# Kernel optimization log

Measured on AMD Instinct MI355X. Metric: run time of the kernel, lower is better.

The kernel has to match this reference:

```python
import jax, jax.numpy as jnp
import numpy as np
from jax import lax

B, C, N = 128, 320, 256
H = W = 16
GROUPS = 5
RATIO = 8
MASK_EPS = 1e-6   # registered buffer 'eps' in the torch module
GN_EPS = 1e-5     # torch GroupNorm default


def setup_inputs() -> dict:
    key = jax.random.key(0)
    ks = jax.random.split(key, 10)
    def rn(k, shape, scale=0.05):
        return jax.random.normal(k, shape, dtype=jnp.float32) * scale
    return {
        "x": jax.random.normal(ks[0], (B, C, N), dtype=jnp.float32),
        "low_cutoff": jnp.float32(0.2),
        "high_cutoff": jnp.float32(0.7),
        "ca_w1": rn(ks[1], (C // RATIO, C)),
        "ca_b1": jnp.zeros((C // RATIO,), jnp.float32),
        "ca_w2": rn(ks[2], (3 * C, C // RATIO)),
        "ca_b2": jnp.zeros((3 * C,), jnp.float32),
        "low_w": rn(ks[3], (C, C, 3, 3)),
        "low_b": jnp.zeros((C,), jnp.float32),
        "low_g": jnp.ones((C,), jnp.float32),
        "low_beta": jnp.zeros((C,), jnp.float32),
        "mid_w": rn(ks[4], (C, C, 3, 3)),
        "mid_b": jnp.zeros((C,), jnp.float32),
        "mid_g": jnp.ones((C,), jnp.float32),
        "mid_beta": jnp.zeros((C,), jnp.float32),
        "high_w": rn(ks[5], (C, C, 3, 3)),
        "high_b": jnp.zeros((C,), jnp.float32),
        "high_g": jnp.ones((C,), jnp.float32),
        "high_beta": jnp.zeros((C,), jnp.float32),
        "sa_w": rn(ks[6], (1, C, 1, 1)),
        "sa_b": jnp.zeros((1,), jnp.float32),
    }


def _conv3x3_gn(y, w, b, gamma, beta):
    # Conv2d(C,C,3,padding=1) -> GroupNorm(5,C)
    out = lax.conv_general_dilated(
        y, w, window_strides=(1, 1), padding='SAME',
        dimension_numbers=('NCHW', 'OIHW', 'NCHW'))
    out = out + b[None, :, None, None]
    b_, c_, h_, w_ = out.shape
    g = out.reshape(b_, GROUPS, c_ // GROUPS, h_, w_)
    mu = g.mean(axis=(2, 3, 4), keepdims=True)
    var = g.var(axis=(2, 3, 4), keepdims=True)
    g = (g - mu) * lax.rsqrt(var + GN_EPS)
    out = g.reshape(b_, c_, h_, w_)
    return out * gamma[None, :, None, None] + beta[None, :, None, None]


def reference(x, low_cutoff, high_cutoff, ca_w1, ca_b1, ca_w2, ca_b2,
              low_w, low_b, low_g, low_beta,
              mid_w, mid_b, mid_g, mid_beta,
              high_w, high_b, high_g, high_beta,
              sa_w, sa_b):
    b, c, n = x.shape
    n_pix = H * W
    # reshape_to_square (N == n_pix here, pad/slice kept for faithfulness)
    if n < n_pix:
        xp = jnp.pad(x, ((0, 0), (0, 0), (0, n_pix - n)))
    else:
        xp = x[:, :, :n_pix]
    x2d = xp.reshape(b, c, H, W)

    # DynamicFrequencyFilter: avgpool over N -> 1x1 conv1d -> relu -> 1x1 conv1d -> sigmoid
    avg = x.mean(axis=-1)                                  # [B, C]
    hcw = jax.nn.relu(avg @ ca_w1.T + ca_b1)               # [B, C//8]
    cw = jax.nn.sigmoid(hcw @ ca_w2.T + ca_b2)             # [B, 3C]
    cw = cw.reshape(b, 3, c, 1, 1)

    # FFT + shifted frequency masks. torch fftshift(dim=None) shifts all dims,
    # but the B/C shifts commute with the (B/C-broadcast) mask multiply and are
    # undone by ifftshift, so shifting only the spatial axes is equivalent.
    fft_feat = jnp.fft.fftshift(jnp.fft.fft2(x2d), axes=(-2, -1))
    yy, xx = jnp.meshgrid(jnp.linspace(-1.0, 1.0, H), jnp.linspace(-1.0, 1.0, W), indexing='ij')
    dist = jnp.sqrt(xx ** 2 + yy ** 2) / np.sqrt(2.0)
    low_mask = jax.nn.sigmoid((low_cutoff - dist) / MASK_EPS)
    mid_mask = jax.nn.sigmoid((dist - low_cutoff) / MASK_EPS) * jax.nn.sigmoid((high_cutoff - dist) / MASK_EPS)
    high_mask = jax.nn.sigmoid((dist - high_cutoff) / MASK_EPS)

    def band(mask):
        return jnp.fft.ifft2(jnp.fft.ifftshift(fft_feat * mask, axes=(-2, -1))).real

    low_feat = _conv3x3_gn(band(low_mask), low_w, low_b, low_g, low_beta) + x2d
    mid_feat = _conv3x3_gn(band(mid_mask), mid_w, mid_b, mid_g, mid_beta) + x2d
    high_feat = _conv3x3_gn(band(high_mask), high_w, high_b, high_g, high_beta) + x2d

    fused = cw[:, 0] * low_feat + cw[:, 1] * mid_feat + cw[:, 2] * high_feat

    # spatial attention: 1x1 conv C->1, sigmoid
    sw = jax.nn.sigmoid(jnp.einsum('bchw,c->bhw', fused, sa_w[0, :, 0, 0])[:, None] + sa_b[0])
    out = (fused * sw).reshape(b, c, n_pix)
    return out[:, :, :n]
```

## Files before the change

### kernel.cpp

```cpp
#include <hip/hip_runtime.h>
#include <math.h>

#define NB 128
#define NC 320
#define NG 5
#define CPG 64
#define NHID 40

typedef short bf16x8 __attribute__((ext_vector_type(8)));
typedef short s16x4  __attribute__((ext_vector_type(4)));
typedef float f32x4  __attribute__((ext_vector_type(4)));

__device__ __forceinline__ float sigf(float x){ return 1.0f/(1.0f+expf(-x)); }

__device__ __forceinline__ unsigned short f2b(float f){
  unsigned u = __float_as_uint(f);
  unsigned r = (u + 0x7fffu + ((u >> 16) & 1u)) >> 16;
  return (unsigned short)r;
}
__device__ __forceinline__ float b2f(unsigned short u){
  return __uint_as_float(((unsigned)u) << 16);
}

__device__ __forceinline__ void gll16(const void* g, void* l){
  __builtin_amdgcn_global_load_lds(
      (const __attribute__((address_space(1))) void*)g,
      (__attribute__((address_space(3))) void*)l, 16, 0, 0);
}

__global__ __launch_bounds__(256) void k_kern(const float* __restrict__ lowc,
                                              const float* __restrict__ highc,
                                              float* __restrict__ kern){
  __shared__ float msh[256];
  __shared__ float cost[16];
  int band = blockIdx.x, t = threadIdx.x;
  float lc = lowc[0], hc = highc[0];
  {
    int a1 = t >> 4, a2 = t & 15;
    const float step = 2.0f / 15.0f;
    float cy = -1.0f + step * (float)a1;
    float cx = -1.0f + step * (float)a2;
    float dist = sqrtf(cx*cx + cy*cy) / 1.41421356237309515f;
    float m = band == 0 ? sigf((lc - dist) * 1e6f)
            : band == 1 ? sigf((dist - lc) * 1e6f) * sigf((hc - dist) * 1e6f)
                        : sigf((dist - hc) * 1e6f);
    msh[t] = m;
  }
  if (t < 16) cost[t] = cosf((float)t * 0.392699081698724154f);
  __syncthreads();
  int d1 = t >> 4, d2 = t & 15;
  float s = 0.f;
  int ang0 = (8*d1 + 8*d2) & 15;
  for (int a1 = 0; a1 < 16; ++a1){
    int ang = (ang0 + a1*d1) & 15;
    #pragma unroll
    for (int a2 = 0; a2 < 16; ++a2){
      s += msh[a1*16 + a2] * cost[ang];
      ang = (ang + d2) & 15;
    }
  }
  kern[band*256 + t] = s * (1.0f/256.0f);
}

__global__ __launch_bounds__(256) void k_gather(const float* __restrict__ kern,
                                                unsigned short* __restrict__ WgT){
  __shared__ float ksh[256];
  int band = blockIdx.x >> 8, p = blockIdx.x & 255, q = threadIdx.x;
  ksh[q] = kern[band*256 + q];
  __syncthreads();
  int d1 = ((p >> 4) - (q >> 4)) & 15;
  int d2 = ((p & 15) - (q & 15)) & 15;
  WgT[(size_t)(band << 16) + (p << 8) + q] = f2b(ksh[(d1 << 4) | d2]);
}

__global__ __launch_bounds__(256) void k_wt2(const float* __restrict__ w0,
                                             const float* __restrict__ w1,
                                             const float* __restrict__ w2,
                                             unsigned short* __restrict__ WAb){
  __shared__ float wsh[2880];
  int band = blockIdx.x / 320, co = blockIdx.x % 320;
  const float* w = band == 0 ? w0 : (band == 1 ? w1 : w2);
  const float* src = w + (size_t)co * 2880;
  for (int i = threadIdx.x; i < 2880; i += 256) wsh[i] = src[i];
  __syncthreads();
  unsigned short* dst = WAb + (size_t)band * 921600;
  for (int g = threadIdx.x; g < 360; g += 256){
    int tap = g / 40, r = g % 40;
    unsigned short tmp[8];
    #pragma unroll
    for (int j = 0; j < 8; ++j) tmp[j] = f2b(wsh[(r*8 + j)*9 + tap]);
    s16x4* o = (s16x4*)(dst + (size_t)g * 2560 + co*8);
    o[0] = *(s16x4*)tmp;
    o[1] = *(s16x4*)(tmp + 4);
  }
}

__global__ __launch_bounds__(256) void k_zerohalo(unsigned short* __restrict__ bandT){
  unsigned short* base = bandT + (size_t)blockIdx.x * 103680;
  for (int i = threadIdx.x; i < 5440; i += 256){
    int idx = i / 80, v = i % 80;
    int r, c;
    if (idx < 18)      { r = 0;        c = idx;      }
    else if (idx < 36) { r = 17;       c = idx - 18; }
    else if (idx < 52) { r = idx - 35; c = 0;        }
    else               { r = idx - 51; c = 17;       }
    s16x4 z = {0,0,0,0};
    *(s16x4*)(base + (size_t)(r*18 + c)*NC + v*4) = z;
  }
}

__global__ __launch_bounds__(256) void k_ca(const float* __restrict__ avg,
                                            const float* __restrict__ w1,
                                            const float* __restrict__ b1,
                                            const float* __restrict__ w2,
                                            const float* __restrict__ b2,
                                            float* __restrict__ cw){
  __shared__ float a[NC];
  __shared__ float h[NHID];
  int b = blockIdx.x, t = threadIdx.x;
  a[t] = avg[b * NC + t];
  if (t < NC - 256) a[256 + t] = avg[b * NC + 256 + t];
  __syncthreads();
  if (t < NHID){
    float s = b1[t];
    for (int i = 0; i < NC; ++i) s += w1[t * NC + i] * a[i];
    h[t] = fmaxf(s, 0.0f);
  }
  __syncthreads();
  for (int o = t; o < 3 * NC; o += 256){
    float s = b2[o];
    for (int i = 0; i < NHID; ++i) s += w2[o * NHID + i] * h[i];
    cw[b * (3 * NC) + o] = sigf(s);
  }
}

__global__ __launch_bounds__(256, 4) void k_bandg3(const float* __restrict__ x,
                                                   const unsigned short* __restrict__ WgT,
                                                   unsigned short* __restrict__ bandT,
                                                   float* __restrict__ avgOut){
  __shared__ unsigned short xt[64*256];
  int tid = threadIdx.x;
  int wgid = (blockIdx.x & 7)*80 + (blockIdx.x >> 3);
  int b = wgid / 5, cq = wgid % 5;
  int cibase = cq * 64;
  size_t rowbase = (size_t)wgid * 64;

  {
    int r = tid >> 2, c0 = (tid & 3) * 64;
    const float* xp = x + (rowbase + r)*256 + c0;
    unsigned short* dp = xt + r*256;
    int sw = (r & 7) << 3;
    float rs = 0.f;
    #pragma unroll
    for (int j = 0; j < 64; j += 4){
      float4 f = *(const float4*)(xp + j);
      rs += f.x + f.y + f.z + f.w;
      unsigned short t4[4] = { f2b(f.x), f2b(f.y), f2b(f.z), f2b(f.w) };
      *(s16x4*)(dp + ((c0 + j) ^ sw)) = *(s16x4*)t4;
    }
    rs += __shfl_down(rs, 1);
    rs += __shfl_down(rs, 2);
    if ((tid & 3) == 0) avgOut[rowbase + r] = rs * (1.0f/256.0f);
  }
  __syncthreads();

  int l  = tid & 63;
  int wq = tid >> 6;
  int cig = l >> 4, lan = l & 15;

  for (int band = 0; band < 3; ++band){
    const unsigned short* Wg = WgT + (size_t)band * 65536;
    unsigned short* bT = bandT + (size_t)band * 13271040;

    f32x4 acc[4][4];
    #pragma unroll
    for (int m = 0; m < 4; ++m)
      #pragma unroll
      for (int n = 0; n < 4; ++n) acc[m][n] = (f32x4){0.f,0.f,0.f,0.f};

    #pragma unroll 2
    for (int ks = 0; ks < 8; ++ks){
      int koff = ks*32 + cig*8;
      bf16x8 a[4], bv[4];
      #pragma unroll
      for (int m = 0; m < 4; ++m){
        int row = m*16 + lan;
        a[m] = *(const bf16x8*)(xt + row*256 + (koff ^ ((row & 7) << 3)));
      }
      #pragma unroll
      for (int n = 0; n < 4; ++n){
        int p = wq*64 + n*16 + lan;
        bv[n] = *(const bf16x8*)(Wg + (size_t)p*256 + koff);
      }
      #pragma unroll
      for (int m = 0; m < 4; ++m)
        #pragma unroll
        for (int n = 0; n < 4; ++n)
          acc[m][n] = __builtin_amdgcn_mfma_f32_16x16x32_bf16(a[m], bv[n], acc[m][n], 0, 0, 0);
    }

    #pragma unroll
    for (int m = 0; m < 4; ++m){
      #pragma unroll
      for (int n = 0; n < 4; ++n){
        int p = wq*64 + n*16 + lan;
        int slot = ((p >> 4) + 1) * 18 + (p & 15) + 1;
        int ci = cibase + m*16 + cig*4;
        unsigned short o[4] = { f2b(acc[m][n][0]), f2b(acc[m][n][1]),
                                f2b(acc[m][n][2]), f2b(acc[m][n][3]) };
        *(s16x4*)(bT + ((size_t)(b*324 + slot))*NC + ci) = *(s16x4*)o;
      }
    }
  }
}

__global__ __launch_bounds__(256, 3) void k_convg(const unsigned short* __restrict__ bandT,
                                                  const unsigned short* __restrict__ WAb,
                                                  const float* __restrict__ bias0,
                                                  const float* __restrict__ bias1,
                                                  const float* __restrict__ bias2,
                                                  unsigned short* __restrict__ convb,
                                                  float* __restrict__ stats_part){
  __shared__ char ldsA[3*10240];
  __shared__ char ldsB[2*11520];
  __shared__ float stw[4][5][2];

  int tid = threadIdx.x;
  int wgid = (blockIdx.x & 7)*192 + (blockIdx.x >> 3);
  int band = wgid / 512; int rem = wgid & 511;
  int b = rem >> 2, ch = (rem >> 1) & 1, ph = rem & 1;

  const unsigned short* bT = bandT + (size_t)band*13271040 + (size_t)b*103680;
  const unsigned short* WA = WAb + (size_t)band*921600;
  const float* bias = band == 0 ? bias0 : (band == 1 ? bias1 : bias2);
  unsigned short* cbp = convb + (size_t)band * 10485760;

  int l = tid & 63, w = tid >> 6;
  int wco = w >> 1, wpx = w & 1;
  int cig = l >> 4, lan = l & 15;
  int cobase = ch*160 + wco*80;
  int px0 = ph*128 + wpx*64;

  int ga0 = tid, ga1 = tid + 256, ga2 = tid + 512;
  int aoff0 = (ga0/160)*2560 + (ga0%160)*8 + ch*1280;
  int aoff1 = (ga1/160)*2560 + (ga1%160)*8 + ch*1280;
  int aoff2 = (ga2/160)*2560 + (ga2%160)*8 + ch*1280;
  int gb0 = tid, gb1 = tid + 256, gb2 = tid + 512;
  int boff0 = (ph*144 + gb0%180)*320 + (gb0/180)*8;
  int boff1 = (ph*144 + gb1%180)*320 + (gb1/180)*8;
  int boff2 = (ph*144 + gb2%180)*320 + (gb2/180)*8;

  int Aread0 = (cig*160 + wco*80 + lan)*16;
  int Bread0 = (cig*180 + (wpx*4 + 1)*18 + lan + 1)*16;

  f32x4 acc[5][4];
  #pragma unroll
  for (int m = 0; m < 5; ++m)
    #pragma unroll
    for (int n = 0; n < 4; ++n) acc[m][n] = (f32x4){0.f,0.f,0.f,0.f};

#define STAGE_A(TAP, CIB, BUF) do { \
    const unsigned short* sA = WA + (size_t)((TAP)*40 + (CIB)*4)*2560; \
    char* dA = ldsA + (BUF)*10240; \
    gll16(sA + aoff0, dA + tid*16); \
    gll16(sA + aoff1, dA + 4096 + tid*16); \
    if (tid < 128) gll16(sA + aoff2, dA + 8192 + tid*16); \
  } while(0)

#define STAGE_B(CN) do { \
    const unsigned short* sB = bT + (CN)*32; \
    char* dB = ldsB + ((CN)&1)*11520; \
    gll16(sB + boff0, dB + tid*16); \
    gll16(sB + boff1, dB + 4096 + tid*16); \
    if (tid < 208) gll16(sB + boff2, dB + 8192 + tid*16); \
  } while(0)

#define VWAIT(N) asm volatile("s_waitcnt vmcnt(" #N ")" ::: "memory")

  STAGE_A(0, 0, 0);
  STAGE_B(0);
  STAGE_A(1, 0, 1);
  VWAIT(2);
  __builtin_amdgcn_s_barrier();

  for (int cib = 0; cib < 10; ++cib){
    #pragma unroll
    for (int tap = 0; tap < 9; ++tap){
      const char* Ab = ldsA + (tap % 3)*10240 + Aread0;
      bf16x8 a0 = *(const bf16x8*)(Ab);
      bf16x8 a1 = *(const bf16x8*)(Ab + 256);
      bf16x8 a2 = *(const bf16x8*)(Ab + 512);
      bf16x8 a3 = *(const bf16x8*)(Ab + 768);
      bf16x8 a4 = *(const bf16x8*)(Ab + 1024);
      const int dhdw = ((tap/3)*18 + (tap%3) - 19)*16;
      const char* Bb = ldsB + (cib & 1)*11520 + Bread0 + dhdw;
      bf16x8 b0 = *(const bf16x8*)(Bb);
      bf16x8 b1 = *(const bf16x8*)(Bb + 288);
      bf16x8 b2 = *(const bf16x8*)(Bb + 576);
      bf16x8 b3 = *(const bf16x8*)(Bb + 864);

      if (tap <= 6){
        STAGE_A(tap + 2, cib, (tap + 2) % 3);
      } else if (cib < 9){
        STAGE_A(tap - 7, cib + 1, (tap + 2) % 3);
      }
      if (tap == 0 && cib < 9) STAGE_B(cib + 1);

      __builtin_amdgcn_s_setprio(1);
      acc[0][0] = __builtin_amdgcn_mfma_f32_16x16x32_bf16(a0, b0, acc[0][0],0,0,0);
      acc[0][1] = __builtin_amdgcn_mfma_f32_16x16x32_bf16(a0, b1, acc[0][1],0,0,0);
      acc[0][2] = __builtin_amdgcn_mfma_f32_16x16x32_bf16(a0, b2, acc[0][2],0,0,0);
      acc[0][3] = __builtin_amdgcn_mfma_f32_16x16x32_bf16(a0, b3, acc[0][3],0,0,0);
      acc[1][0] = __builtin_amdgcn_mfma_f32_16x16x32_bf16(a1, b0, acc[1][0],0,0,0);
      acc[1][1] = __builtin_amdgcn_mfma_f32_16x16x32_bf16(a1, b1, acc[1][1],0,0,0);
      acc[1][2] = __builtin_amdgcn_mfma_f32_16x16x32_bf16(a1, b2, acc[1][2],0,0,0);
      acc[1][3] = __builtin_amdgcn_mfma_f32_16x16x32_bf16(a1, b3, acc[1][3],0,0,0);
      acc[2][0] = __builtin_amdgcn_mfma_f32_16x16x32_bf16(a2, b0, acc[2][0],0,0,0);
      acc[2][1] = __builtin_amdgcn_mfma_f32_16x16x32_bf16(a2, b1, acc[2][1],0,0,0);
      acc[2][2] = __builtin_amdgcn_mfma_f32_16x16x32_bf16(a2, b2, acc[2][2],0,0,0);
      acc[2][3] = __builtin_amdgcn_mfma_f32_16x16x32_bf16(a2, b3, acc[2][3],0,0,0);
      acc[3][0] = __builtin_amdgcn_mfma_f32_16x16x32_bf16(a3, b0, acc[3][0],0,0,0);
      acc[3][1] = __builtin_amdgcn_mfma_f32_16x16x32_bf16(a3, b1, acc[3][1],0,0,0);
      acc[3][2] = __builtin_amdgcn_mfma_f32_16x16x32_bf16(a3, b2, acc[3][2],0,0,0);
      acc[3][3] = __builtin_amdgcn_mfma_f32_16x16x32_bf16(a3, b3, acc[3][3],0,0,0);
      acc[4][0] = __builtin_amdgcn_mfma_f32_16x16x32_bf16(a4, b0, acc[4][0],0,0,0);
      acc[4][1] = __builtin_amdgcn_mfma_f32_16x16x32_bf16(a4, b1, acc[4][1],0,0,0);
      acc[4][2] = __builtin_amdgcn_mfma_f32_16x16x32_bf16(a4, b2, acc[4][2],0,0,0);
      acc[4][3] = __builtin_amdgcn_mfma_f32_16x16x32_bf16(a4, b3, acc[4][3],0,0,0);
      __builtin_amdgcn_s_setprio(0);

      if (tap <= 1){
        if (cib < 9) { VWAIT(5); } else { VWAIT(2); }
      } else if (tap == 7){
        if (cib < 9) { VWAIT(2); } else { VWAIT(0); }
      } else if (tap == 8){
        if (cib < 9) { VWAIT(2); }
      } else {
        VWAIT(2);
      }
      if (!(cib == 9 && tap == 8)) __builtin_amdgcn_s_barrier();
    }
  }
#undef STAGE_A
#undef STAGE_B
#undef VWAIT

  #pragma unroll
  for (int m = 0; m < 5; ++m)
    #pragma unroll
    for (int r = 0; r < 4; ++r){
      float bvs = bias[cobase + m*16 + cig*4 + r];
      #pragma unroll
      for (int n = 0; n < 4; ++n) acc[m][n][r] += bvs;
    }

  #pragma unroll
  for (int m = 0; m < 5; ++m){
    float s = 0.f, q = 0.f;
    #pragma unroll
    for (int n = 0; n < 4; ++n)
      #pragma unroll
      for (int r = 0; r < 4; ++r){ float v = acc[m][n][r]; s += v; q += v*v; }
    #pragma unroll
    for (int o = 32; o > 0; o >>= 1){ s += __shfl_xor(s, o); q += __shfl_xor(q, o); }
    if (l == 0){ stw[w][m][0] = s; stw[w][m][1] = q; }
  }

  #pragma unroll
  for (int m = 0; m < 5; ++m)
    #pragma unroll
    for (int r = 0; r < 4; ++r){
      int co = cobase + m*16 + cig*4 + r;
      unsigned short* op = cbp + ((size_t)(b*NC + co))*256 + px0 + lan;
      #pragma unroll
      for (int n = 0; n < 4; ++n) op[n*16] = f2b(acc[m][n][r]);
    }

  __syncthreads();
  if (tid < 6){
    int gl = tid >> 1, comp = tid & 1;
    int g = ch*2 + gl;
    float t = 0.f;
    for (int w2 = 0; w2 < 4; ++w2)
      #pragma unroll
      for (int m = 0; m < 5; ++m)
        if (((ch*160 + (w2 >> 1)*80 + m*16) >> 6) == g) t += stw[w2][m][comp];
    stats_part[((size_t)(band*NB + b)*NG + g)*8 + ch*4 + ph*2 + comp] = t;
  }
}

__global__ __launch_bounds__(512) void k_fuse3(const unsigned short* __restrict__ cb0,
                                               const unsigned short* __restrict__ cb1,
                                               const unsigned short* __restrict__ cb2,
                                               const float* __restrict__ x,
                                               const float* __restrict__ stats_part,
                                               const float* __restrict__ g0, const float* __restrict__ be0,
                                               const float* __restrict__ g1, const float* __restrict__ be1,
                                               const float* __restrict__ g2, const float* __restrict__ be2,
                                               const float* __restrict__ cw,
                                               const float* __restrict__ saw,
                                               const float* __restrict__ sab,
                                               float* __restrict__ out){
  __shared__ unsigned short fl[NC*128];
  __shared__ float mu_s[3][NG], rs_s[3][NG], sh[4][128];
  int b = blockIdx.x >> 1, half = blockIdx.x & 1;
  int tid = threadIdx.x;
  if (tid < 15){
    int band = tid / 5, g = tid % 5;
    const float* sp = stats_part + ((size_t)(band*NB + b)*NG + g)*8;
    float s = 0.f, q = 0.f;
    if (g <= 2){ s += sp[0] + sp[2]; q += sp[1] + sp[3]; }
    if (g >= 2){ s += sp[4] + sp[6]; q += sp[5] + sp[7]; }
    float mu = s * (1.f/16384.f);
    float var = q * (1.f/16384.f) - mu*mu;
    mu_s[band][g] = mu; rs_s[band][g] = rsqrtf(var + 1e-5f);
  }
  __syncthreads();

  int p = tid & 127, cs = tid >> 7;
  int px = half*128 + p;
  float sacc = 0.f;
  const float* cwb = cw + b*960;
  for (int ci = cs; ci < NC; ci += 4){
    int g = ci >> 6;
    size_t idx = ((size_t)(b*NC + ci))*256 + px;
    float xv = x[idx];
    float f =
      cwb[ci      ] * ((b2f(cb0[idx]) - mu_s[0][g])*rs_s[0][g]*g0[ci] + be0[ci] + xv) +
      cwb[320 + ci] * ((b2f(cb1[idx]) - mu_s[1][g])*rs_s[1][g]*g1[ci] + be1[ci] + xv) +
      cwb[640 + ci] * ((b2f(cb2[idx]) - mu_s[2][g])*rs_s[2][g]*g2[ci] + be2[ci] + xv);
    fl[ci*128 + p] = f2b(f);
    sacc += f * saw[ci];
  }
  sh[cs][p] = sacc;
  __syncthreads();
  if (tid < 128) sh[0][tid] = sigf(sh[0][tid] + sh[1][tid] + sh[2][tid] + sh[3][tid] + sab[0]);
  __syncthreads();
  float swv = sh[0][p];
  for (int ci = cs; ci < NC; ci += 4){
    size_t idx = ((size_t)(b*NC + ci))*256 + px;
    out[idx] = b2f(fl[ci*128 + p]) * swv;
  }
}

extern "C" void kernel_launch(void* const* d_in, const int* in_sizes, int n_in,
                              void* d_out, int out_size, void* d_ws, size_t ws_size,
                              hipStream_t stream){
  (void)in_sizes; (void)n_in; (void)out_size; (void)ws_size;
  const float* x     = (const float*)d_in[0];
  const float* lowc  = (const float*)d_in[1];
  const float* highc = (const float*)d_in[2];
  const float* ca_w1 = (const float*)d_in[3];
  const float* ca_b1 = (const float*)d_in[4];
  const float* ca_w2 = (const float*)d_in[5];
  const float* ca_b2 = (const float*)d_in[6];
  const float* conv_w[3] = {(const float*)d_in[7],  (const float*)d_in[11], (const float*)d_in[15]};
  const float* conv_b[3] = {(const float*)d_in[8],  (const float*)d_in[12], (const float*)d_in[16]};
  const float* gn_g[3]   = {(const float*)d_in[9],  (const float*)d_in[13], (const float*)d_in[17]};
  const float* gn_be[3]  = {(const float*)d_in[10], (const float*)d_in[14], (const float*)d_in[18]};
  const float* sa_w = (const float*)d_in[19];
  const float* sa_b = (const float*)d_in[20];
  float* out = (float*)d_out;

  char* base = (char*)d_ws;
  float*          kern  = (float*)base;
  unsigned short* WgT   = (unsigned short*)(base + 4096);
  unsigned short* WAb   = (unsigned short*)(base + 397312);
  unsigned short* bandT = (unsigned short*)(base + 5926912);
  unsigned short* cbb   = (unsigned short*)(base + 85553152);
  float*          cw    = (float*)(base + 148467712);
  float*          avg   = (float*)(base + 148959232);
  float*          stats = (float*)(base + 149123072);
  unsigned short* cb0 = cbb;
  unsigned short* cb1 = cbb + 10485760;
  unsigned short* cb2 = cbb + 20971520;

  k_kern    <<<3,    256, 0, stream>>>(lowc, highc, kern);
  k_gather  <<<768,  256, 0, stream>>>(kern, WgT);
  k_wt2     <<<960,  256, 0, stream>>>(conv_w[0], conv_w[1], conv_w[2], WAb);
  k_zerohalo<<<384,  256, 0, stream>>>(bandT);

  k_bandg3<<<640, 256, 0, stream>>>(x, WgT, bandT, avg);
  k_ca    <<<NB,  256, 0, stream>>>(avg, ca_w1, ca_b1, ca_w2, ca_b2, cw);

  k_convg<<<1536, 256, 0, stream>>>(bandT, WAb, conv_b[0], conv_b[1], conv_b[2],
                                    cbb, stats);

  k_fuse3<<<256, 512, 0, stream>>>(cb0, cb1, cb2, x, stats,
                                   gn_g[0], gn_be[0], gn_g[1], gn_be[1], gn_g[2], gn_be[2],
                                   cw, sa_w, sa_b, out);
}
```

Baseline: 280.1 us.

## Enlarge conv tile to cover all 256 pixels per workgroup, halving grid

The implicit-GEMM conv kernel now computes every pixel of an image per workgroup instead of splitting pixels into two halves. Each wave holds 5x8 accumulator tiles, and the B tile in LDS grows to the full 18x18 padded image. This halves how often the weight (A) tiles are loaded and staged per output, and it drops the per-half stats partials. In exchange it raises register pressure (occupancy bound lowered from 3 to 2), increases LDS use, and halves the grid to 768 workgroups, which may leave fewer waves to hide latency.

```diff
diff --git a/kernel.cpp b/kernel.cpp
--- a/kernel.cpp
+++ b/kernel.cpp
@@ -214,7 +214,7 @@
   }
 }
 
-__global__ __launch_bounds__(256, 3) void k_convg(const unsigned short* __restrict__ bandT,
+__global__ __launch_bounds__(256, 2) void k_convg(const unsigned short* __restrict__ bandT,
                                                   const unsigned short* __restrict__ WAb,
                                                   const float* __restrict__ bias0,
                                                   const float* __restrict__ bias1,
@@ -222,13 +222,13 @@
                                                   unsigned short* __restrict__ convb,
                                                   float* __restrict__ stats_part){
   __shared__ char ldsA[3*10240];
-  __shared__ char ldsB[2*11520];
+  __shared__ char ldsB[2*20736];
   __shared__ float stw[4][5][2];
 
   int tid = threadIdx.x;
-  int wgid = (blockIdx.x & 7)*192 + (blockIdx.x >> 3);
-  int band = wgid / 512; int rem = wgid & 511;
-  int b = rem >> 2, ch = (rem >> 1) & 1, ph = rem & 1;
+  int wgid = (blockIdx.x & 7)*96 + (blockIdx.x >> 3);
+  int band = wgid >> 8; int rem = wgid & 255;
+  int b = rem >> 1, ch = rem & 1;
 
   const unsigned short* bT = bandT + (size_t)band*13271040 + (size_t)b*103680;
   const unsigned short* WA = WAb + (size_t)band*921600;
@@ -239,25 +239,31 @@
   int wco = w >> 1, wpx = w & 1;
   int cig = l >> 4, lan = l & 15;
   int cobase = ch*160 + wco*80;
-  int px0 = ph*128 + wpx*64;
+  int px0 = wpx*128;
 
   int ga0 = tid, ga1 = tid + 256, ga2 = tid + 512;
   int aoff0 = (ga0/160)*2560 + (ga0%160)*8 + ch*1280;
   int aoff1 = (ga1/160)*2560 + (ga1%160)*8 + ch*1280;
   int aoff2 = (ga2/160)*2560 + (ga2%160)*8 + ch*1280;
-  int gb0 = tid, gb1 = tid + 256, gb2 = tid + 512;
-  int boff0 = (ph*144 + gb0%180)*320 + (gb0/180)*8;
-  int boff1 = (ph*144 + gb1%180)*320 + (gb1/180)*8;
-  int boff2 = (ph*144 + gb2%180)*320 + (gb2/180)*8;
+  int boff0, boff1, boff2, boff3, boff4, boffR;
+  {
+    int g;
+    g = tid;        boff0 = (g%324)*320 + (g/324)*8;
+    g = tid + 256;  boff1 = (g%324)*320 + (g/324)*8;
+    g = tid + 512;  boff2 = (g%324)*320 + (g/324)*8;
+    g = tid + 768;  boff3 = (g%324)*320 + (g/324)*8;
+    g = tid + 1024; boff4 = (g%324)*320 + (g/324)*8;
+    g = tid + 1280; boffR = (g%324)*320 + (g/324)*8;
+  }
 
   int Aread0 = (cig*160 + wco*80 + lan)*16;
-  int Bread0 = (cig*180 + (wpx*4 + 1)*18 + lan + 1)*16;
-
-  f32x4 acc[5][4];
+  int Bread0 = (cig*324 + (wpx*8 + 1)*18 + lan + 1)*16;
+
+  f32x4 acc[5][8];
   #pragma unroll
   for (int m = 0; m < 5; ++m)
     #pragma unroll
-    for (int n = 0; n < 4; ++n) acc[m][n] = (f32x4){0.f,0.f,0.f,0.f};
+    for (int n = 0; n < 8; ++n) acc[m][n] = (f32x4){0.f,0.f,0.f,0.f};
 
 #define STAGE_A(TAP, CIB, BUF) do { \
     const unsigned short* sA = WA + (size_t)((TAP)*40 + (CIB)*4)*2560; \
@@ -269,10 +275,13 @@
 
 #define STAGE_B(CN) do { \
     const unsigned short* sB = bT + (CN)*32; \
-    char* dB = ldsB + ((CN)&1)*11520; \
+    char* dB = ldsB + ((CN)&1)*20736; \
     gll16(sB + boff0, dB + tid*16); \
     gll16(sB + boff1, dB + 4096 + tid*16); \
-    if (tid < 208) gll16(sB + boff2, dB + 8192 + tid*16); \
+    gll16(sB + boff2, dB + 8192 + tid*16); \
+    gll16(sB + boff3, dB + 12288 + tid*16); \
+    gll16(sB + boff4, dB + 16384 + tid*16); \
+    if (tid < 16) gll16(sB + boffR, dB + 20480 + tid*16); \
   } while(0)
 
 #define VWAIT(N) asm volatile("s_waitcnt vmcnt(" #N ")" ::: "memory")
@@ -293,11 +302,15 @@
       bf16x8 a3 = *(const bf16x8*)(Ab + 768);
       bf16x8 a4 = *(const bf16x8*)(Ab + 1024);
       const int dhdw = ((tap/3)*18 + (tap%3) - 19)*16;
-      const char* Bb = ldsB + (cib & 1)*11520 + Bread0 + dhdw;
+      const char* Bb = ldsB + (cib & 1)*20736 + Bread0 + dhdw;
       bf16x8 b0 = *(const bf16x8*)(Bb);
       bf16x8 b1 = *(const bf16x8*)(Bb + 288);
       bf16x8 b2 = *(const bf16x8*)(Bb + 576);
       bf16x8 b3 = *(const bf16x8*)(Bb + 864);
+      bf16x8 b4 = *(const bf16x8*)(Bb + 1152);
+      bf16x8 b5 = *(const bf16x8*)(Bb + 1440);
+      bf16x8 b6 = *(const bf16x8*)(Bb + 1728);
+      bf16x8 b7 = *(const bf16x8*)(Bb + 2016);
 
       if (tap <= 6){
         STAGE_A(tap + 2, cib, (tap + 2) % 3);
@@ -307,30 +320,21 @@
       if (tap == 0 && cib < 9) STAGE_B(cib + 1);
 
       __builtin_amdgcn_s_setprio(1);
-      acc[0][0] = __builtin_amdgcn_mfma_f32_16x16x32_bf16(a0, b0, acc[0][0],0,0,0);
-      acc[0][1] = __builtin_amdgcn_mfma_f32_16x16x32_bf16(a0, b1, acc[0][1],0,0,0);
-      acc[0][2] = __builtin_amdgcn_mfma_f32_16x16x32_bf16(a0, b2, acc[0][2],0,0,0);
-      acc[0][3] = __builtin_amdgcn_mfma_f32_16x16x32_bf16(a0, b3, acc[0][3],0,0,0);
-      acc[1][0] = __builtin_amdgcn_mfma_f32_16x16x32_bf16(a1, b0, acc[1][0],0,0,0);
-      acc[1][1] = __builtin_amdgcn_mfma_f32_16x16x32_bf16(a1, b1, acc[1][1],0,0,0);
-      acc[1][2] = __builtin_amdgcn_mfma_f32_16x16x32_bf16(a1, b2, acc[1][2],0,0,0);
-      acc[1][3] = __builtin_amdgcn_mfma_f32_16x16x32_bf16(a1, b3, acc[1][3],0,0,0);
-      acc[2][0] = __builtin_amdgcn_mfma_f32_16x16x32_bf16(a2, b0, acc[2][0],0,0,0);
-      acc[2][1] = __builtin_amdgcn_mfma_f32_16x16x32_bf16(a2, b1, acc[2][1],0,0,0);
-      acc[2][2] = __builtin_amdgcn_mfma_f32_16x16x32_bf16(a2, b2, acc[2][2],0,0,0);
-      acc[2][3] = __builtin_amdgcn_mfma_f32_16x16x32_bf16(a2, b3, acc[2][3],0,0,0);
-      acc[3][0] = __builtin_amdgcn_mfma_f32_16x16x32_bf16(a3, b0, acc[3][0],0,0,0);
-      acc[3][1] = __builtin_amdgcn_mfma_f32_16x16x32_bf16(a3, b1, acc[3][1],0,0,0);
-      acc[3][2] = __builtin_amdgcn_mfma_f32_16x16x32_bf16(a3, b2, acc[3][2],0,0,0);
-      acc[3][3] = __builtin_amdgcn_mfma_f32_16x16x32_bf16(a3, b3, acc[3][3],0,0,0);
-      acc[4][0] = __builtin_amdgcn_mfma_f32_16x16x32_bf16(a4, b0, acc[4][0],0,0,0);
-      acc[4][1] = __builtin_amdgcn_mfma_f32_16x16x32_bf16(a4, b1, acc[4][1],0,0,0);
-      acc[4][2] = __builtin_amdgcn_mfma_f32_16x16x32_bf16(a4, b2, acc[4][2],0,0,0);
-      acc[4][3] = __builtin_amdgcn_mfma_f32_16x16x32_bf16(a4, b3, acc[4][3],0,0,0);
+#define MM8(M, AV) \
+      acc[M][0]=__builtin_amdgcn_mfma_f32_16x16x32_bf16(AV, b0, acc[M][0],0,0,0); \
+      acc[M][1]=__builtin_amdgcn_mfma_f32_16x16x32_bf16(AV, b1, acc[M][1],0,0,0); \
+      acc[M][2]=__builtin_amdgcn_mfma_f32_16x16x32_bf16(AV, b2, acc[M][2],0,0,0); \
+      acc[M][3]=__builtin_amdgcn_mfma_f32_16x16x32_bf16(AV, b3, acc[M][3],0,0,0); \
+      acc[M][4]=__builtin_amdgcn_mfma_f32_16x16x32_bf16(AV, b4, acc[M][4],0,0,0); \
+      acc[M][5]=__builtin_amdgcn_mfma_f32_16x16x32_bf16(AV, b5, acc[M][5],0,0,0); \
+      acc[M][6]=__builtin_amdgcn_mfma_f32_16x16x32_bf16(AV, b6, acc[M][6],0,0,0); \
+      acc[M][7]=__builtin_amdgcn_mfma_f32_16x16x32_bf16(AV, b7, acc[M][7],0,0,0);
+      MM8(0, a0) MM8(1, a1) MM8(2, a2) MM8(3, a3) MM8(4, a4)
+#undef MM8
       __builtin_amdgcn_s_setprio(0);
 
       if (tap <= 1){
-        if (cib < 9) { VWAIT(5); } else { VWAIT(2); }
+        if (cib < 9) { VWAIT(7); } else { VWAIT(2); }
       } else if (tap == 7){
         if (cib < 9) { VWAIT(2); } else { VWAIT(0); }
       } else if (tap == 8){
@@ -351,14 +355,14 @@
     for (int r = 0; r < 4; ++r){
       float bvs = bias[cobase + m*16 + cig*4 + r];
       #pragma unroll
-      for (int n = 0; n < 4; ++n) acc[m][n][r] += bvs;
+      for (int n = 0; n < 8; ++n) acc[m][n][r] += bvs;
     }
 
   #pragma unroll
   for (int m = 0; m < 5; ++m){
     float s = 0.f, q = 0.f;
     #pragma unroll
-    for (int n = 0; n < 4; ++n)
+    for (int n = 0; n < 8; ++n)
       #pragma unroll
       for (int r = 0; r < 4; ++r){ float v = acc[m][n][r]; s += v; q += v*v; }
     #pragma unroll
@@ -373,7 +377,7 @@
       int co = cobase + m*16 + cig*4 + r;
       unsigned short* op = cbp + ((size_t)(b*NC + co))*256 + px0 + lan;
       #pragma unroll
-      for (int n = 0; n < 4; ++n) op[n*16] = f2b(acc[m][n][r]);
+      for (int n = 0; n < 8; ++n) op[n*16] = f2b(acc[m][n][r]);
     }
 
   __syncthreads();
@@ -385,7 +389,7 @@
       #pragma unroll
       for (int m = 0; m < 5; ++m)
         if (((ch*160 + (w2 >> 1)*80 + m*16) >> 6) == g) t += stw[w2][m][comp];
-    stats_part[((size_t)(band*NB + b)*NG + g)*8 + ch*4 + ph*2 + comp] = t;
+    stats_part[((size_t)(band*NB + b)*NG + g)*4 + ch*2 + comp] = t;
   }
 }
 
@@ -407,10 +411,10 @@
   int tid = threadIdx.x;
   if (tid < 15){
     int band = tid / 5, g = tid % 5;
-    const float* sp = stats_part + ((size_t)(band*NB + b)*NG + g)*8;
+    const float* sp = stats_part + ((size_t)(band*NB + b)*NG + g)*4;
     float s = 0.f, q = 0.f;
-    if (g <= 2){ s += sp[0] + sp[2]; q += sp[1] + sp[3]; }
-    if (g >= 2){ s += sp[4] + sp[6]; q += sp[5] + sp[7]; }
+    if (g <= 2){ s += sp[0]; q += sp[1]; }
+    if (g >= 2){ s += sp[2]; q += sp[3]; }
     float mu = s * (1.f/16384.f);
     float var = q * (1.f/16384.f) - mu*mu;
     mu_s[band][g] = mu; rs_s[band][g] = rsqrtf(var + 1e-5f);
@@ -483,8 +487,8 @@
   k_bandg3<<<640, 256, 0, stream>>>(x, WgT, bandT, avg);
   k_ca    <<<NB,  256, 0, stream>>>(avg, ca_w1, ca_b1, ca_w2, ca_b2, cw);
 
-  k_convg<<<1536, 256, 0, stream>>>(bandT, WAb, conv_b[0], conv_b[1], conv_b[2],
-                                    cbb, stats);
+  k_convg<<<768, 256, 0, stream>>>(bandT, WAb, conv_b[0], conv_b[1], conv_b[2],
+                                   cbb, stats);
 
   k_fuse3<<<256, 512, 0, stream>>>(cb0, cb1, cb2, x, stats,
                                    gn_g[0], gn_be[0], gn_g[1], gn_be[1], gn_g[2], gn_be[2],
```

New measurement: 304.8 us. 8.8% more time.

## Merge prep kernels, fold halo zeroing and channel attention into consumers

Applied to the files above, without the earlier changes.

Merges the mask-kernel, gather and weight-transpose prologue kernels into one launch; the mask kernel is now recomputed redundantly in each gather block instead of read from workspace. Halo zeroing moves into the band kernel and the channel-attention MLP moves into the fuse kernel, which recomputes it for each of the two half-blocks per batch. This cuts the launch count from eight to four, at the price of redundant work per block and a serial 40-thread MLP prologue in the fuse kernel.

```diff
diff --git a/kernel.cpp b/kernel.cpp
--- a/kernel.cpp
+++ b/kernel.cpp
@@ -28,109 +28,70 @@
       (__attribute__((address_space(3))) void*)l, 16, 0, 0);
 }
 
-__global__ __launch_bounds__(256) void k_kern(const float* __restrict__ lowc,
+__global__ __launch_bounds__(256) void k_prep(const float* __restrict__ lowc,
                                               const float* __restrict__ highc,
-                                              float* __restrict__ kern){
+                                              const float* __restrict__ w0,
+                                              const float* __restrict__ w1,
+                                              const float* __restrict__ w2,
+                                              unsigned short* __restrict__ WgT,
+                                              unsigned short* __restrict__ WAb){
   __shared__ float msh[256];
   __shared__ float cost[16];
-  int band = blockIdx.x, t = threadIdx.x;
-  float lc = lowc[0], hc = highc[0];
-  {
-    int a1 = t >> 4, a2 = t & 15;
-    const float step = 2.0f / 15.0f;
-    float cy = -1.0f + step * (float)a1;
-    float cx = -1.0f + step * (float)a2;
-    float dist = sqrtf(cx*cx + cy*cy) / 1.41421356237309515f;
-    float m = band == 0 ? sigf((lc - dist) * 1e6f)
-            : band == 1 ? sigf((dist - lc) * 1e6f) * sigf((hc - dist) * 1e6f)
-                        : sigf((dist - hc) * 1e6f);
-    msh[t] = m;
-  }
-  if (t < 16) cost[t] = cosf((float)t * 0.392699081698724154f);
-  __syncthreads();
-  int d1 = t >> 4, d2 = t & 15;
-  float s = 0.f;
-  int ang0 = (8*d1 + 8*d2) & 15;
-  for (int a1 = 0; a1 < 16; ++a1){
-    int ang = (ang0 + a1*d1) & 15;
-    #pragma unroll
-    for (int a2 = 0; a2 < 16; ++a2){
-      s += msh[a1*16 + a2] * cost[ang];
-      ang = (ang + d2) & 15;
-    }
-  }
-  kern[band*256 + t] = s * (1.0f/256.0f);
-}
-
-__global__ __launch_bounds__(256) void k_gather(const float* __restrict__ kern,
-                                                unsigned short* __restrict__ WgT){
   __shared__ float ksh[256];
-  int band = blockIdx.x >> 8, p = blockIdx.x & 255, q = threadIdx.x;
-  ksh[q] = kern[band*256 + q];
-  __syncthreads();
-  int d1 = ((p >> 4) - (q >> 4)) & 15;
-  int d2 = ((p & 15) - (q & 15)) & 15;
-  WgT[(size_t)(band << 16) + (p << 8) + q] = f2b(ksh[(d1 << 4) | d2]);
-}
-
-__global__ __launch_bounds__(256) void k_wt2(const float* __restrict__ w0,
-                                             const float* __restrict__ w1,
-                                             const float* __restrict__ w2,
-                                             unsigned short* __restrict__ WAb){
   __shared__ float wsh[2880];
-  int band = blockIdx.x / 320, co = blockIdx.x % 320;
-  const float* w = band == 0 ? w0 : (band == 1 ? w1 : w2);
-  const float* src = w + (size_t)co * 2880;
-  for (int i = threadIdx.x; i < 2880; i += 256) wsh[i] = src[i];
-  __syncthreads();
-  unsigned short* dst = WAb + (size_t)band * 921600;
-  for (int g = threadIdx.x; g < 360; g += 256){
-    int tap = g / 40, r = g % 40;
-    unsigned short tmp[8];
-    #pragma unroll
-    for (int j = 0; j < 8; ++j) tmp[j] = f2b(wsh[(r*8 + j)*9 + tap]);
-    s16x4* o = (s16x4*)(dst + (size_t)g * 2560 + co*8);
-    o[0] = *(s16x4*)tmp;
-    o[1] = *(s16x4*)(tmp + 4);
-  }
-}
-
-__global__ __launch_bounds__(256) void k_zerohalo(unsigned short* __restrict__ bandT){
-  unsigned short* base = bandT + (size_t)blockIdx.x * 103680;
-  for (int i = threadIdx.x; i < 5440; i += 256){
-    int idx = i / 80, v = i % 80;
-    int r, c;
-    if (idx < 18)      { r = 0;        c = idx;      }
-    else if (idx < 36) { r = 17;       c = idx - 18; }
-    else if (idx < 52) { r = idx - 35; c = 0;        }
-    else               { r = idx - 51; c = 17;       }
-    s16x4 z = {0,0,0,0};
-    *(s16x4*)(base + (size_t)(r*18 + c)*NC + v*4) = z;
-  }
-}
-
-__global__ __launch_bounds__(256) void k_ca(const float* __restrict__ avg,
-                                            const float* __restrict__ w1,
-                                            const float* __restrict__ b1,
-                                            const float* __restrict__ w2,
-                                            const float* __restrict__ b2,
-                                            float* __restrict__ cw){
-  __shared__ float a[NC];
-  __shared__ float h[NHID];
-  int b = blockIdx.x, t = threadIdx.x;
-  a[t] = avg[b * NC + t];
-  if (t < NC - 256) a[256 + t] = avg[b * NC + 256 + t];
-  __syncthreads();
-  if (t < NHID){
-    float s = b1[t];
-    for (int i = 0; i < NC; ++i) s += w1[t * NC + i] * a[i];
-    h[t] = fmaxf(s, 0.0f);
-  }
-  __syncthreads();
-  for (int o = t; o < 3 * NC; o += 256){
-    float s = b2[o];
-    for (int i = 0; i < NHID; ++i) s += w2[o * NHID + i] * h[i];
-    cw[b * (3 * NC) + o] = sigf(s);
+  int bid = blockIdx.x, t = threadIdx.x;
+
+  if (bid < 768){
+    int band = bid >> 8, p = bid & 255;
+    float lc = lowc[0], hc = highc[0];
+    {
+      int a1 = t >> 4, a2 = t & 15;
+      const float step = 2.0f / 15.0f;
+      float cy = -1.0f + step * (float)a1;
+      float cx = -1.0f + step * (float)a2;
+      float dist = sqrtf(cx*cx + cy*cy) / 1.41421356237309515f;
+      float m = band == 0 ? sigf((lc - dist) * 1e6f)
+              : band == 1 ? sigf((dist - lc) * 1e6f) * sigf((hc - dist) * 1e6f)
+                          : sigf((dist - hc) * 1e6f);
+      msh[t] = m;
+    }
+    if (t < 16) cost[t] = cosf((float)t * 0.392699081698724154f);
+    __syncthreads();
+    {
+      int d1 = t >> 4, d2 = t & 15;
+      float s = 0.f;
+      int ang0 = (8*d1 + 8*d2) & 15;
+      for (int a1 = 0; a1 < 16; ++a1){
+        int ang = (ang0 + a1*d1) & 15;
+        #pragma unroll
+        for (int a2 = 0; a2 < 16; ++a2){
+          s += msh[a1*16 + a2] * cost[ang];
+          ang = (ang + d2) & 15;
+        }
+      }
+      ksh[t] = s * (1.0f/256.0f);
+    }
+    __syncthreads();
+    int d1 = ((p >> 4) - (t >> 4)) & 15;
+    int d2 = ((p & 15) - (t & 15)) & 15;
+    WgT[(size_t)(band << 16) + (p << 8) + t] = f2b(ksh[(d1 << 4) | d2]);
+  } else {
+    int bid2 = bid - 768;
+    int band = bid2 / 320, co = bid2 % 320;
+    const float* w = band == 0 ? w0 : (band == 1 ? w1 : w2);
+    const float* src = w + (size_t)co * 2880;
+    for (int i = t; i < 2880; i += 256) wsh[i] = src[i];
+    __syncthreads();
+    unsigned short* dst = WAb + (size_t)band * 921600;
+    for (int g = t; g < 360; g += 256){
+      int tap = g / 40, r = g % 40;
+      unsigned short tmp[8];
+      #pragma unroll
+      for (int j = 0; j < 8; ++j) tmp[j] = f2b(wsh[(r*8 + j)*9 + tap]);
+      s16x4* o = (s16x4*)(dst + (size_t)g * 2560 + co*8);
+      o[0] = *(s16x4*)tmp;
+      o[1] = *(s16x4*)(tmp + 4);
+    }
   }
 }
 
@@ -161,6 +122,19 @@
     rs += __shfl_down(rs, 1);
     rs += __shfl_down(rs, 2);
     if ((tid & 3) == 0) avgOut[rowbase + r] = rs * (1.0f/256.0f);
+  }
+
+  for (int i = tid; i < 3264; i += 256){
+    int band = i / 1088, r = i % 1088;
+    int si = r >> 4, cg = r & 15;
+    int rr, cc;
+    if (si < 18)      { rr = 0;        cc = si;      }
+    else if (si < 36) { rr = 17;       cc = si - 18; }
+    else if (si < 52) { rr = si - 35;  cc = 0;       }
+    else              { rr = si - 51;  cc = 17;      }
+    s16x4 z = {0,0,0,0};
+    *(s16x4*)(bandT + (size_t)band*13271040 +
+              ((size_t)(b*324 + rr*18 + cc))*NC + cibase + cg*4) = z;
   }
   __syncthreads();
 
@@ -397,16 +371,24 @@
                                                const float* __restrict__ g0, const float* __restrict__ be0,
                                                const float* __restrict__ g1, const float* __restrict__ be1,
                                                const float* __restrict__ g2, const float* __restrict__ be2,
-                                               const float* __restrict__ cw,
+                                               const float* __restrict__ avg,
+                                               const float* __restrict__ caw1,
+                                               const float* __restrict__ cab1,
+                                               const float* __restrict__ caw2,
+                                               const float* __restrict__ cab2,
                                                const float* __restrict__ saw,
                                                const float* __restrict__ sab,
                                                float* __restrict__ out){
   __shared__ unsigned short fl[NC*128];
   __shared__ float mu_s[3][NG], rs_s[3][NG], sh[4][128];
+  __shared__ float avs[NC], hsh[NHID], cws[3*NC];
   int b = blockIdx.x >> 1, half = blockIdx.x & 1;
   int tid = threadIdx.x;
-  if (tid < 15){
-    int band = tid / 5, g = tid % 5;
+
+  if (tid < NC) avs[tid] = avg[b*NC + tid];
+  else if (tid >= 496 && tid < 511){
+    int t2 = tid - 496;
+    int band = t2 / 5, g = t2 % 5;
     const float* sp = stats_part + ((size_t)(band*NB + b)*NG + g)*8;
     float s = 0.f, q = 0.f;
     if (g <= 2){ s += sp[0] + sp[2]; q += sp[1] + sp[3]; }
@@ -416,19 +398,33 @@
     mu_s[band][g] = mu; rs_s[band][g] = rsqrtf(var + 1e-5f);
   }
   __syncthreads();
+  if (tid < NHID){
+    float s = cab1[tid];
+    const float* wr = caw1 + tid*NC;
+    for (int i = 0; i < NC; ++i) s += wr[i] * avs[i];
+    hsh[tid] = fmaxf(s, 0.0f);
+  }
+  __syncthreads();
+  for (int o = tid; o < 3*NC; o += 512){
+    float s = cab2[o];
+    const float* wr = caw2 + o*NHID;
+    #pragma unroll
+    for (int i = 0; i < NHID; ++i) s += wr[i] * hsh[i];
+    cws[o] = sigf(s);
+  }
+  __syncthreads();
 
   int p = tid & 127, cs = tid >> 7;
   int px = half*128 + p;
   float sacc = 0.f;
-  const float* cwb = cw + b*960;
   for (int ci = cs; ci < NC; ci += 4){
     int g = ci >> 6;
     size_t idx = ((size_t)(b*NC + ci))*256 + px;
     float xv = x[idx];
     float f =
-      cwb[ci      ] * ((b2f(cb0[idx]) - mu_s[0][g])*rs_s[0][g]*g0[ci] + be0[ci] + xv) +
-      cwb[320 + ci] * ((b2f(cb1[idx]) - mu_s[1][g])*rs_s[1][g]*g1[ci] + be1[ci] + xv) +
-      cwb[640 + ci] * ((b2f(cb2[idx]) - mu_s[2][g])*rs_s[2][g]*g2[ci] + be2[ci] + xv);
+      cws[ci      ] * ((b2f(cb0[idx]) - mu_s[0][g])*rs_s[0][g]*g0[ci] + be0[ci] + xv) +
+      cws[320 + ci] * ((b2f(cb1[idx]) - mu_s[1][g])*rs_s[1][g]*g1[ci] + be1[ci] + xv) +
+      cws[640 + ci] * ((b2f(cb2[idx]) - mu_s[2][g])*rs_s[2][g]*g2[ci] + be2[ci] + xv);
     fl[ci*128 + p] = f2b(f);
     sacc += f * saw[ci];
   }
@@ -463,30 +459,26 @@
   float* out = (float*)d_out;
 
   char* base = (char*)d_ws;
-  float*          kern  = (float*)base;
   unsigned short* WgT   = (unsigned short*)(base + 4096);
   unsigned short* WAb   = (unsigned short*)(base + 397312);
   unsigned short* bandT = (unsigned short*)(base + 5926912);
   unsigned short* cbb   = (unsigned short*)(base + 85553152);
-  float*          cw    = (float*)(base + 148467712);
   float*          avg   = (float*)(base + 148959232);
   float*          stats = (float*)(base + 149123072);
   unsigned short* cb0 = cbb;
   unsigned short* cb1 = cbb + 10485760;
   unsigned short* cb2 = cbb + 20971520;
 
-  k_kern    <<<3,    256, 0, stream>>>(lowc, highc, kern);
-  k_gather  <<<768,  256, 0, stream>>>(kern, WgT);
-  k_wt2     <<<960,  256, 0, stream>>>(conv_w[0], conv_w[1], conv_w[2], WAb);
-  k_zerohalo<<<384,  256, 0, stream>>>(bandT);
+  k_prep  <<<1728, 256, 0, stream>>>(lowc, highc, conv_w[0], conv_w[1], conv_w[2],
+                                     WgT, WAb);
 
   k_bandg3<<<640, 256, 0, stream>>>(x, WgT, bandT, avg);
-  k_ca    <<<NB,  256, 0, stream>>>(avg, ca_w1, ca_b1, ca_w2, ca_b2, cw);
 
   k_convg<<<1536, 256, 0, stream>>>(bandT, WAb, conv_b[0], conv_b[1], conv_b[2],
                                     cbb, stats);
 
   k_fuse3<<<256, 512, 0, stream>>>(cb0, cb1, cb2, x, stats,
                                    gn_g[0], gn_be[0], gn_g[1], gn_be[1], gn_g[2], gn_be[2],
-                                   cw, sa_w, sa_b, out);
-}
+                                   avg, ca_w1, ca_b1, ca_w2, ca_b2,
+                                   sa_w, sa_b, out);
+}
```

After: 265.2 us. 5.3% less time.
